# Kernel tuning notes

Measured on AMD Instinct MI355X. Metric: run time of the kernel, lower is better.

The kernel has to match this reference:

```python
import jax, jax.numpy as jnp
import numpy as np

DIM, NH, WS, SR, CTS = 256, 8, 8, 4, 2
HD = DIM // NH
SCALE = HD ** -0.5

def _linear(x, w, b=None):
    y = x @ w.T
    return y + b if b is not None else y

def _ln(x, g, b, eps=1e-5):
    m = jnp.mean(x, -1, keepdims=True)
    v = jnp.mean((x - m) ** 2, -1, keepdims=True)
    return (x - m) / jnp.sqrt(v + eps) * g + b

def _mlp(x, w1, b1, w2, b2):
    return _linear(jax.nn.gelu(_linear(x, w1, b1), approximate=False), w2, b2)

def _pos_emb_rank3(seq_len, w1, b1, w2):
    # PosEmbMLPSwinv1D with rank=3: coords on cube_root(seq) grid, normalized
    s = int(round(seq_len ** (1.0 / 3.0)))
    c = (jnp.arange(s, dtype=jnp.float32) - s // 2) / (s // 2)
    grid = jnp.stack(jnp.meshgrid(c, c, c, indexing='ij'))      # (3,s,s,s)
    tbl = grid.reshape(3, -1).T                                 # (s^3,3)
    return _linear(jax.nn.relu(_linear(tbl, w1, b1)), w2)[None]  # (1,s^3,dim)

def _rel_bias_3d(ws, w1, b1, w2, n_global):
    # PosEmbMLPSwinv3D: CPB-MLP bias over 3D relative coords, 16*sigmoid, zero-pad for carrier tokens
    r = jnp.arange(-(ws - 1), ws, dtype=jnp.float32)
    tbl = jnp.stack(jnp.meshgrid(r, r, r, indexing='ij'), axis=-1) / (ws - 1)
    tbl = tbl * 8.0
    tbl = jnp.sign(tbl) * jnp.log2(jnp.abs(tbl) + 1.0) / np.log2(8.0)
    table = _linear(jax.nn.relu(_linear(tbl.reshape(-1, 3), w1, b1)), w2)  # ((2ws-1)^3, NH)
    coords = jnp.stack(jnp.meshgrid(jnp.arange(ws), jnp.arange(ws), jnp.arange(ws), indexing='ij'))
    cf = coords.reshape(3, -1)
    rel = (cf[:, :, None] - cf[:, None, :]).transpose(1, 2, 0) + (ws - 1)  # (P,P,3)
    idx = rel[..., 0] * (2 * ws - 1) ** 2 + rel[..., 1] * (2 * ws - 1) + rel[..., 2]
    P = ws ** 3
    bias = table[idx.reshape(-1)].reshape(P, P, NH).transpose(2, 0, 1)
    bias = 16.0 * jax.nn.sigmoid(bias)
    return jnp.pad(bias, ((0, 0), (n_global, 0), (n_global, 0)))[None]  # (1,NH,P+g,P+g)

def _win_attn(x, qkv_w, qkv_b, proj_w, proj_b, bias):
    B, N, C = x.shape
    qkv = _linear(x, qkv_w, qkv_b).reshape(B, N, 3, NH, HD).transpose(2, 0, 3, 1, 4)
    q, k, v = qkv[0], qkv[1], qkv[2]
    attn = jax.nn.softmax(jnp.einsum('bhnd,bhmd->bhnm', q, k) * SCALE + bias, axis=-1)
    out = jnp.einsum('bhnm,bhmd->bhnd', attn, v).transpose(0, 2, 1, 3).reshape(B, N, C)
    return _linear(out, proj_w, proj_b)

def _ct_dewindow(ct, W, H, D, ws):
    bs, _, N = ct.shape
    c = ct.reshape(bs, W // ws, H // ws, D // ws, ws, ws, ws, N)
    c = c.transpose(0, 7, 1, 3, 5, 2, 4, 6).reshape(bs, N, W * H * D)
    return c.transpose(0, 2, 1)

def _ct_window(ct, W, H, D, ws):
    bs, _, N = ct.shape
    c = ct.reshape(bs, H // ws, ws, W // ws, ws, D // ws, ws, N)
    return c.transpose(0, 1, 3, 5, 2, 4, 6, 7)

def setup_inputs() -> dict:
    key = jax.random.key(0)
    ks = jax.random.split(key, 48)
    B0 = 1
    nw = SR ** 3
    def w(k, *s):
        return jax.random.normal(k, s, jnp.float32) * 0.02
    def b(k, *s):
        return jax.random.normal(k, s, jnp.float32) * 0.01
    d4 = 4 * DIM
    return {
        'x': jax.random.normal(ks[0], (B0 * nw, WS ** 3, DIM), jnp.float32),
        'ct': jax.random.normal(ks[1], (B0, (CTS * SR) ** 3, DIM), jnp.float32),
        'pe_w1': w(ks[2], 512, 3), 'pe_b1': b(ks[3], 512), 'pe_w2': w(ks[4], DIM, 512),
        'hpe_w1': w(ks[5], 512, 3), 'hpe_b1': b(ks[6], 512), 'hpe_w2': w(ks[7], DIM, 512),
        'hat_n1_g': jnp.ones((DIM,), jnp.float32), 'hat_n1_b': jnp.zeros((DIM,), jnp.float32),
        'hat_qkv_w': w(ks[8], 3 * DIM, DIM), 'hat_qkv_b': b(ks[9], 3 * DIM),
        'hat_proj_w': w(ks[10], DIM, DIM), 'hat_proj_b': b(ks[11], DIM),
        'hat_cpb_w1': w(ks[12], 512, 3), 'hat_cpb_b1': b(ks[13], 512), 'hat_cpb_w2': w(ks[14], NH, 512),
        'hat_n2_g': jnp.ones((DIM,), jnp.float32), 'hat_n2_b': jnp.zeros((DIM,), jnp.float32),
        'hat_fc1_w': w(ks[15], d4, DIM), 'hat_fc1_b': b(ks[16], d4),
        'hat_fc2_w': w(ks[17], DIM, d4), 'hat_fc2_b': b(ks[18], DIM),
        'n1_g': jnp.ones((DIM,), jnp.float32), 'n1_b': jnp.zeros((DIM,), jnp.float32),
        'qkv_w': w(ks[19], 3 * DIM, DIM), 'qkv_b': b(ks[20], 3 * DIM),
        'proj_w': w(ks[21], DIM, DIM), 'proj_b': b(ks[22], DIM),
        'cpb_w1': w(ks[23], 512, 3), 'cpb_b1': b(ks[24], 512), 'cpb_w2': w(ks[25], NH, 512),
        'n2_g': jnp.ones((DIM,), jnp.float32), 'n2_b': jnp.zeros((DIM,), jnp.float32),
        'fc1_w': w(ks[26], d4, DIM), 'fc1_b': b(ks[27], d4),
        'fc2_w': w(ks[28], DIM, d4), 'fc2_b': b(ks[29], DIM),
    }

def reference(x, ct, pe_w1, pe_b1, pe_w2, hpe_w1, hpe_b1, hpe_w2,
              hat_n1_g, hat_n1_b, hat_qkv_w, hat_qkv_b, hat_proj_w, hat_proj_b,
              hat_cpb_w1, hat_cpb_b1, hat_cpb_w2, hat_n2_g, hat_n2_b,
              hat_fc1_w, hat_fc1_b, hat_fc2_w, hat_fc2_b,
              n1_g, n1_b, qkv_w, qkv_b, proj_w, proj_b,
              cpb_w1, cpb_b1, cpb_w2, n2_g, n2_b, fc1_w, fc1_b, fc2_w, fc2_b):
    Bg, Ng, Hg = ct.shape
    G = CTS * SR  # carrier-token global cube side
    x = x + _pos_emb_rank3(x.shape[1], pe_w1, pe_b1, pe_w2)
    # carrier-token global attention (hierarchical path)
    ct = _ct_dewindow(ct, G, G, G, CTS)
    ct = ct + _pos_emb_rank3(ct.shape[1], hpe_w1, hpe_b1, hpe_w2)
    hat_bias = _rel_bias_3d(G, hat_cpb_w1, hat_cpb_b1, hat_cpb_w2, 0)
    ct = ct + _win_attn(_ln(ct, hat_n1_g, hat_n1_b), hat_qkv_w, hat_qkv_b, hat_proj_w, hat_proj_b, hat_bias)
    ct = ct + _mlp(_ln(ct, hat_n2_g, hat_n2_b), hat_fc1_w, hat_fc1_b, hat_fc2_w, hat_fc2_b)
    ct_w = _ct_window(ct, G, G, G, CTS).reshape(x.shape[0], -1, Hg)
    # windowed attention over [carrier tokens ; window tokens]
    x = jnp.concatenate([ct_w, x], axis=1)
    bias = _rel_bias_3d(WS, cpb_w1, cpb_b1, cpb_w2, CTS ** 3)
    x = x + _win_attn(_ln(x, n1_g, n1_b), qkv_w, qkv_b, proj_w, proj_b, bias)
    x = x + _mlp(_ln(x, n2_g, n2_b), fc1_w, fc1_b, fc2_w, fc2_b)
    split = x.shape[1] - WS ** 3
    ctr, x = x[:, :split], x[:, split:]
    return x, ctr.reshape(Bg, Ng, Hg)
```

## Files before the change

kernel.cpp:

```cpp
#include <hip/hip_runtime.h>
#include <hip/hip_bf16.h>
#include <math.h>

typedef __hip_bfloat16 bf16;

#define SCALE_QK 0.17677669529663687f

__device__ __forceinline__ float b2f(bf16 v){ return __bfloat162float(v); }
__device__ __forceinline__ bf16  f2b(float v){ return __float2bfloat16(v); }
__device__ __forceinline__ short bfs(float x){ bf16 b = f2b(x); short s; __builtin_memcpy(&s, &b, 2); return s; }

struct __align__(16) bf16x8 { bf16 v[8]; };
struct __align__(8)  bf16x4 { bf16 v[4]; };

typedef __attribute__((ext_vector_type(8))) short sh8;
typedef __attribute__((ext_vector_type(4))) short sh4;
typedef __attribute__((ext_vector_type(4))) float f4;

#if defined(__has_builtin)
#if __has_builtin(__builtin_amdgcn_mfma_f32_16x16x16bf16_1k)
#define HAS_MFMA16 1
#else
#define HAS_MFMA16 0
#endif
// ... 64 lines not shown
    int i = t / 225, r = t - i * 225, j = r / 15, k = r - j * 15;
    float x0 = cpb_coord(i), x1 = cpb_coord(j), x2 = cpb_coord(k);
    float h = x0 * w1[tid*3+0] + x1 * w1[tid*3+1] + x2 * w1[tid*3+2] + b1[tid];
    hid[tid] = fmaxf(h, 0.f);
    __syncthreads();
    int h8 = tid >> 6, lane = tid & 63;
    float p = 0.f;
    for (int jj = lane; jj < 512; jj += 64) p += hid[jj] * w2[h8*512 + jj];
    for (int off = 32; off; off >>= 1) p += __shfl_down(p, off);
    if (lane == 0) tab[t * 8 + h8] = p;
}

__global__ __launch_bounds__(256) void biasbuild_k(const float* __restrict__ taba, float* __restrict__ biasQa,
                                                   const float* __restrict__ tabb, float* __restrict__ biasQb) {
    const float* tab = blockIdx.y ? tabb : taba;
    float* biasQ     = blockIdx.y ? biasQb : biasQa;
    int idx = blockIdx.x * 256 + threadIdx.x;
    int h = idx >> 18, rem = idx & 262143;
    int q = rem >> 9, k = rem & 511;
    int qx = q >> 6, qy = (q >> 3) & 7, qz = q & 7;
    int kx = k >> 6, ky = (k >> 3) & 7, kz = k & 7;
    int tidx = ((qx - kx + 7) * 15 + (qy - ky + 7)) * 15 + (qz - kz + 7);
    float v = tab[tidx * 8 + h];
    float b = 16.f / (1.f + __expf(-v));
    biasQ[idx] = (b - 24.0f) * 1.4426950408889634f;
}

__global__ __launch_bounds__(256) void ct0ln_k(const float* __restrict__ ct_in,
                                               const float* __restrict__ hpe,
                                               const float* __restrict__ g,
                                               const float* __restrict__ b,
                                               float* __restrict__ ct0,
                                               bf16* __restrict__ lnout) {
    int u = blockIdx.x, c = threadIdx.x;
    int a = u >> 7, cc = (u >> 5) & 3, e = (u >> 4) & 1, bb = (u >> 2) & 3, d = (u >> 1) & 1, f = u & 1;
    int t = a * 128 + bb * 32 + cc * 8 + d * 4 + e * 2 + f;
    float x = ct_in[(size_t)t * 256 + c] + hpe[(size_t)u * 256 + c];
    ct0[(size_t)u * 256 + c] = x;
    float s = x, s2 = x * x;
    for (int off = 32; off; off >>= 1) { s += __shfl_down(s, off); s2 += __shfl_down(s2, off); }
    __shared__ float red[8];
    int wid = c >> 6, lane = c & 63;
    if (lane == 0) { red[wid] = s; red[wid + 4] = s2; }
    __syncthreads();
    if (c == 0) { red[0] = red[0] + red[1] + red[2] + red[3]; red[4] = red[4] + red[5] + red[6] + red[7]; }
    __syncthreads();
    float mean = red[0] * (1.f / 256.f);
    float var  = fmaxf(red[4] * (1.f / 256.f) - mean * mean, 0.f);
    float rstd = rsqrtf(var + 1e-5f);
    lnout[(size_t)u * 256 + c] = f2b((x - mean) * rstd * g[c] + b[c]);
}

__global__ __launch_bounds__(256) void ln_k(const float* __restrict__ in,
                                            const float* __restrict__ g,
                                            const float* __restrict__ b,
                                            bf16* __restrict__ out) {
    int row = blockIdx.x, c = threadIdx.x;
    float x = in[(size_t)row * 256 + c];
    float s = x, s2 = x * x;
    for (int off = 32; off; off >>= 1) { s += __shfl_down(s, off); s2 += __shfl_down(s2, off); }
    __shared__ float red[8];
    int wid = c >> 6, lane = c & 63;
    if (lane == 0) { red[wid] = s; red[wid + 4] = s2; }
    __syncthreads();
    if (c == 0) { red[0] = red[0] + red[1] + red[2] + red[3]; red[4] = red[4] + red[5] + red[6] + red[7]; }
    __syncthreads();
    float mean = red[0] * (1.f / 256.f);
    float var  = fmaxf(red[4] * (1.f / 256.f) - mean * mean, 0.f);
    float rstd = rsqrtf(var + 1e-5f);
    out[(size_t)row * 256 + c] = f2b((x - mean) * rstd * g[c] + b[c]);
}

template <int MODE>
__global__ __launch_bounds__(256) void gemm_k(const bf16* __restrict__ A,
                                              const bf16* __restrict__ W,
                                              const float* __restrict__ bias,
                                              int M, int N, int K,
                                              float* __restrict__ res,
                                              bf16* __restrict__ outb) {
    __shared__ short As[128 * 40];
    __shared__ short Ws[128 * 40];
    int m0 = blockIdx.y * 128, n0 = blockIdx.x * 128;
    int tid = threadIdx.x;
    int lane = tid & 63, wave = tid >> 6;
    int quad = lane >> 4, m16 = lane & 15;
    int wm = (wave & 1) * 64, wn = (wave >> 1) * 64;
    int arow = tid >> 2, acol = (tid & 3) * 8;

    f4 acc[4][4];
    #pragma unroll
    for (int i = 0; i < 4; i++)
        #pragma unroll
        for (int j = 0; j < 4; j++) acc[i][j] = (f4){0.f, 0.f, 0.f, 0.f};

    for (int k0 = 0; k0 < K; k0 += 32) {
        sh8 a0 = *reinterpret_cast<const sh8*>(A + (size_t)(m0 + arow) * K + k0 + acol);
        sh8 a1 = *reinterpret_cast<const sh8*>(A + (size_t)(m0 + arow + 64) * K + k0 + acol);
        sh8 w0 = *reinterpret_cast<const sh8*>(W + (size_t)(n0 + arow) * K + k0 + acol);
        sh8 w1 = *reinterpret_cast<const sh8*>(W + (size_t)(n0 + arow + 64) * K + k0 + acol);
        __syncthreads();
        *reinterpret_cast<sh8*>(&As[arow * 40 + acol])        = a0;
        *reinterpret_cast<sh8*>(&As[(arow + 64) * 40 + acol]) = a1;
        *reinterpret_cast<sh8*>(&Ws[arow * 40 + acol])        = w0;
        *reinterpret_cast<sh8*>(&Ws[(arow + 64) * 40 + acol]) = w1;
        __syncthreads();
        sh8 af[4], bf[4];
        #pragma unroll
        for (int mi = 0; mi < 4; mi++)
            af[mi] = *reinterpret_cast<const sh8*>(&As[(wm + mi * 16 + m16) * 40 + quad * 8]);
        #pragma unroll
        for (int ni = 0; ni < 4; ni++)
            bf[ni] = *reinterpret_cast<const sh8*>(&Ws[(wn + ni * 16 + m16) * 40 + quad * 8]);
        #pragma unroll
        for (int mi = 0; mi < 4; mi++)
            #pragma unroll
            for (int ni = 0; ni < 4; ni++)
                acc[mi][ni] = __builtin_amdgcn_mfma_f32_16x16x32_bf16(af[mi], bf[ni], acc[mi][ni], 0, 0, 0);
    }
    (void)M;

    #pragma unroll
    for (int mi = 0; mi < 4; mi++) {
        #pragma unroll
        for (int r = 0; r < 4; r++) {
            int gm = m0 + wm + mi * 16 + quad * 4 + r;
            #pragma unroll
            for (int ni = 0; ni < 4; ni++) {
                int gn = n0 + wn + ni * 16 + m16;
                float v = acc[mi][ni][r];
                if constexpr (MODE != 3) v += bias[gn];
                if constexpr (MODE == 2)      res[(size_t)gm * N + gn] += v;
                else if constexpr (MODE == 3) res[(size_t)gm * N + gn] = v;
                else if constexpr (MODE == 1) outb[(size_t)gm * N + gn] = f2b(0.5f * v * (1.0f + erff(v * 0.70710678118654752f)));
                else                          outb[(size_t)gm * N + gn] = f2b(v);
            }
        }
    }
}

__global__ __launch_bounds__(512) void gemmln_k(const bf16* __restrict__ A,
                                                const bf16* __restrict__ W,
                                                const float* __restrict__ bias,
                                                float* __restrict__ xcat,
                                                const float* __restrict__ g,
                                                const float* __restrict__ b,
                                                bf16* __restrict__ outb) {
    __shared__ short As[128 * 40];
    __shared__ short Ws[256 * 40];
    __shared__ float redS[128 * 4];
    __shared__ float redQ[128 * 4];
    __shared__ float stat[128 * 2];
    int m0 = blockIdx.x * 128;
    int tid = threadIdx.x;
    int lane = tid & 63, wave = tid >> 6;
    int quad = lane >> 4, m16 = lane & 15;
    int wm = (wave >> 2) * 64, wn = (wave & 3) * 64;
    int arow = tid >> 2, acol = (tid & 3) * 8;

    f4 acc[4][4];
    #pragma unroll
    for (int i = 0; i < 4; i++)
        #pragma unroll
        for (int j = 0; j < 4; j++) acc[i][j] = (f4){0.f, 0.f, 0.f, 0.f};

    for (int k0 = 0; k0 < 256; k0 += 32) {
        sh8 a0 = *reinterpret_cast<const sh8*>(A + (size_t)(m0 + arow) * 256 + k0 + acol);
        sh8 w0 = *reinterpret_cast<const sh8*>(W + (size_t)arow * 256 + k0 + acol);
        sh8 w1 = *reinterpret_cast<const sh8*>(W + (size_t)(arow + 128) * 256 + k0 + acol);
        __syncthreads();
        *reinterpret_cast<sh8*>(&As[arow * 40 + acol])         = a0;
        *reinterpret_cast<sh8*>(&Ws[arow * 40 + acol])         = w0;
        *reinterpret_cast<sh8*>(&Ws[(arow + 128) * 40 + acol]) = w1;
        __syncthreads();
        sh8 af[4], bf[4];
        #pragma unroll
        for (int mi = 0; mi < 4; mi++)
            af[mi] = *reinterpret_cast<const sh8*>(&As[(wm + mi * 16 + m16) * 40 + quad * 8]);
        #pragma unroll
        for (int ni = 0; ni < 4; ni++)
            bf[ni] = *reinterpret_cast<const sh8*>(&Ws[(wn + ni * 16 + m16) * 40 + quad * 8]);
        #pragma unroll
        for (int mi = 0; mi < 4; mi++)
            #pragma unroll
            for (int ni = 0; ni < 4; ni++)
                acc[mi][ni] = __builtin_amdgcn_mfma_f32_16x16x32_bf16(af[mi], bf[ni], acc[mi][ni], 0, 0, 0);
    }

    #pragma unroll
    for (int mi = 0; mi < 4; mi++) {
        #pragma unroll
        for (int r = 0; r < 4; r++) {
            int lr = wm + mi * 16 + quad * 4 + r;
            int gm = m0 + lr;
            float ps = 0.f, pq = 0.f;
            #pragma unroll
            for (int ni = 0; ni < 4; ni++) {
                int gc = wn + ni * 16 + m16;
                float v = acc[mi][ni][r] + bias[gc] + xcat[(size_t)gm * 256 + gc];
                acc[mi][ni][r] = v;
                ps += v; pq += v * v;
            }
            ps += __shfl_xor(ps, 1); pq += __shfl_xor(pq, 1);
            ps += __shfl_xor(ps, 2); pq += __shfl_xor(pq, 2);
            ps += __shfl_xor(ps, 4); pq += __shfl_xor(pq, 4);
            ps += __shfl_xor(ps, 8); pq += __shfl_xor(pq, 8);
            if (m16 == 0) { redS[lr * 4 + (wave & 3)] = ps; redQ[lr * 4 + (wave & 3)] = pq; }
        }
    }
    __syncthreads();
    if (tid < 128) {
        float s = redS[tid * 4] + redS[tid * 4 + 1] + redS[tid * 4 + 2] + redS[tid * 4 + 3];
        float q = redQ[tid * 4] + redQ[tid * 4 + 1] + redQ[tid * 4 + 2] + redQ[tid * 4 + 3];
        float mean = s * (1.f / 256.f);
        float var  = fmaxf(q * (1.f / 256.f) - mean * mean, 0.f);
        stat[tid * 2]     = mean;
        stat[tid * 2 + 1] = rsqrtf(var + 1e-5f);
    }
    __syncthreads();
    #pragma unroll
    for (int mi = 0; mi < 4; mi++) {
        #pragma unroll
        for (int r = 0; r < 4; r++) {
            int lr = wm + mi * 16 + quad * 4 + r;
            int gm = m0 + lr;
            float mean = stat[lr * 2], rstd = stat[lr * 2 + 1];
            #pragma unroll
            for (int ni = 0; ni < 4; ni++) {
                int gc = wn + ni * 16 + m16;
                float v = acc[mi][ni][r];
                xcat[(size_t)gm * 256 + gc] = v;
                outb[(size_t)gm * 256 + gc] = f2b((v - mean) * rstd * g[gc] + b[gc]);
            }
        }
    }
}

__global__ __launch_bounds__(256) void gemmsplit_k(const bf16* __restrict__ A,
                                                   const bf16* __restrict__ W,
                                                   const float* __restrict__ bias,
                                                   int K,
                                                   const float* __restrict__ res,
                                                   float* __restrict__ out) {
    __shared__ short As[128 * 40];
    __shared__ short Ws[128 * 40];
    int m0 = blockIdx.y * 128, n0 = blockIdx.x * 128;
    int tid = threadIdx.x;
    int lane = tid & 63, wave = tid >> 6;
    int quad = lane >> 4, m16 = lane & 15;
    int wm = (wave & 1) * 64, wn = (wave >> 1) * 64;
    int arow = tid >> 2, acol = (tid & 3) * 8;

    f4 acc[4][4];
    #pragma unroll
    for (int i = 0; i < 4; i++)
        #pragma unroll
        for (int j = 0; j < 4; j++) acc[i][j] = (f4){0.f, 0.f, 0.f, 0.f};

    for (int k0 = 0; k0 < K; k0 += 32) {
        sh8 a0 = *reinterpret_cast<const sh8*>(A + (size_t)(m0 + arow) * K + k0 + acol);
        sh8 a1 = *reinterpret_cast<const sh8*>(A + (size_t)(m0 + arow + 64) * K + k0 + acol);
        sh8 w0 = *reinterpret_cast<const sh8*>(W + (size_t)(n0 + arow) * K + k0 + acol);
        sh8 w1 = *reinterpret_cast<const sh8*>(W + (size_t)(n0 + arow + 64) * K + k0 + acol);
        __syncthreads();
        *reinterpret_cast<sh8*>(&As[arow * 40 + acol])        = a0;
        *reinterpret_cast<sh8*>(&As[(arow + 64) * 40 + acol]) = a1;
        *reinterpret_cast<sh8*>(&Ws[arow * 40 + acol])        = w0;
        *reinterpret_cast<sh8*>(&Ws[(arow + 64) * 40 + acol]) = w1;
        __syncthreads();
        sh8 af[4], bf[4];
        #pragma unroll
        for (int mi = 0; mi < 4; mi++)
            af[mi] = *reinterpret_cast<const sh8*>(&As[(wm + mi * 16 + m16) * 40 + quad * 8]);
        #pragma unroll
        for (int ni = 0; ni < 4; ni++)
            bf[ni] = *reinterpret_cast<const sh8*>(&Ws[(wn + ni * 16 + m16) * 40 + quad * 8]);
        #pragma unroll
        for (int mi = 0; mi < 4; mi++)
            #pragma unroll
            for (int ni = 0; ni < 4; ni++)
                acc[mi][ni] = __builtin_amdgcn_mfma_f32_16x16x32_bf16(af[mi], bf[ni], acc[mi][ni], 0, 0, 0);
    }

    #pragma unroll
    for (int mi = 0; mi < 4; mi++) {
        #pragma unroll
        for (int r = 0; r < 4; r++) {
            int gm = m0 + wm + mi * 16 + quad * 4 + r;
            int w = gm / 520, p = gm - w * 520;
            size_t drow = (p >= 8) ? (size_t)(w * 512 + p - 8) : (size_t)(32768 + w * 8 + p);
            #pragma unroll
            for (int ni = 0; ni < 4; ni++) {
                int gn = n0 + wn + ni * 16 + m16;
                float v = acc[mi][ni][r] + bias[gn] + res[(size_t)gm * 256 + gn];
                out[drow * 256 + gn] = v;
            }
        }
    }
}

#define VSTR 548
#define SC2   0.25503575360579045f
#define CNB  (-34.62468098133512f)
#define NEGB (-1.0e30f)
__global__ __launch_bounds__(512) void flash_k(const bf16* __restrict__ qkv,
                                               const float* __restrict__ biasQ,
                                               bf16* __restrict__ out,
                                               int N, int glob) {
    int wh = blockIdx.x, w = wh >> 3, h = wh & 7;
    int qs = blockIdx.y, QS = gridDim.y;
    int tid = threadIdx.x;
    int lane = tid & 63, wave = tid >> 6;
    int quad = lane >> 4, qcol = lane & 15;
    const int NT32 = (N + 31) & ~31;

    __shared__ bf16 Vt[32 * VSTR];
#if !HAS_MFMA16
    __shared__ float Ps[8][16 * 17];
#endif

    for (int i = tid; i < NT32 * 4; i += 512) {
        int tok = i >> 2, seg = i & 3;
        if (tok < N) {
            const bf16* vp = qkv + ((size_t)(w * N + tok)) * 768 + 512 + h * 32 + seg * 8;
            bf16x8 vv = *reinterpret_cast<const bf16x8*>(vp);
            #pragma unroll
            for (int e = 0; e < 8; e++) Vt[(seg * 8 + e) * VSTR + tok] = vv.v[e];
        } else {
            bf16 z = f2b(0.f);
            #pragma unroll
            for (int e = 0; e < 8; e++) Vt[(seg * 8 + e) * VSTR + tok] = z;
        }
    }
    __syncthreads();

    const bf16* qbase = qkv + ((size_t)w * N) * 768 + h * 32;
    const bf16* kbase = qbase + 256;
    int nqt = (N + 15) >> 4, nkt = NT32 >> 5;
    int nun = (nqt + 1) >> 1;

    for (int u = wave * QS + qs; u < nun; u += 8 * QS) {
        bool hasB = (2 * u + 1 < nqt);
        int qA = u * 32 + qcol;
        int qB = qA + 16;
        int qrA = (qA < N) ? qA : (N - 1);
        int qrB = (qB < N) ? qB : (N - 1);
        sh8 qfA = *reinterpret_cast<const sh8*>(qbase + (size_t)qrA * 768 + quad * 8);
        sh8 qfB = *reinterpret_cast<const sh8*>(qbase + (size_t)qrB * 768 + quad * 8);
        f4 O0A = {0.f,0.f,0.f,0.f}, O1A = {0.f,0.f,0.f,0.f};
        f4 O0B = {0.f,0.f,0.f,0.f}, O1B = {0.f,0.f,0.f,0.f};
        float lA = 0.f, lB = 0.f;
        bool vA = (qA >= glob) && (qA < N);
        bool vB = (qB >= glob) && (qB < N);
        const float* browA = biasQ + (((size_t)h << 9) + (size_t)(vA ? (qA - glob) : 0)) * 512 - glob;
        const float* browB = biasQ + (((size_t)h << 9) + (size_t)(vB ? (qB - glob) : 0)) * 512 - glob;

        sh8 kf0, kf1;
        {
            int k0 = qcol, k1 = 16 + qcol;
            kf0 = *reinterpret_cast<const sh8*>(kbase + (size_t)((k0 < N) ? k0 : (N - 1)) * 768 + quad * 8);
            kf1 = *reinterpret_cast<const sh8*>(kbase + (size_t)((k1 < N) ? k1 : (N - 1)) * 768 + quad * 8);
        }

        for (int kt = 0; kt < nkt; kt++) {
            int bt = kt * 32;
            sh8 c0 = kf0, c1 = kf1;
            if (kt + 1 < nkt) {
                int n0 = bt + 32 + qcol, n1 = bt + 48 + qcol;
                kf0 = *reinterpret_cast<const sh8*>(kbase + (size_t)((n0 < N) ? n0 : (N - 1)) * 768 + quad * 8);
                kf1 = *reinterpret_cast<const sh8*>(kbase + (size_t)((n1 < N) ? n1 : (N - 1)) * 768 + quad * 8);
            }
            f4 z = {0.f, 0.f, 0.f, 0.f};
            f4 s0A = __builtin_amdgcn_mfma_f32_16x16x32_bf16(c0, qfA, z, 0, 0, 0);
            f4 s1A = __builtin_amdgcn_mfma_f32_16x16x32_bf16(c1, qfA, z, 0, 0, 0);
            f4 s0B = z, s1B = z;
            if (hasB) {
                s0B = __builtin_amdgcn_mfma_f32_16x16x32_bf16(c0, qfB, z, 0, 0, 0);
                s1B = __builtin_amdgcn_mfma_f32_16x16x32_bf16(c1, qfB, z, 0, 0, 0);
            }

            int tg0 = bt + quad * 4, tg1 = bt + 16 + quad * 4;
            bool val0 = tg0 < N, val1 = tg1 < N;
            f4 bb0A, bb1A;
            if (!val0)                    bb0A = (f4){NEGB, NEGB, NEGB, NEGB};
            else if (vA && tg0 >= glob)   bb0A = *reinterpret_cast<const f4*>(browA + tg0);
            else                          bb0A = (f4){CNB, CNB, CNB, CNB};
            if (!val1)                    bb1A = (f4){NEGB, NEGB, NEGB, NEGB};
            else if (vA && tg1 >= glob)   bb1A = *reinterpret_cast<const f4*>(browA + tg1);
            else                          bb1A = (f4){CNB, CNB, CNB, CNB};

            float pA[8];
            #pragma unroll
            for (int r = 0; r < 4; r++) {
                pA[r]     = EXP2(fmaf(s0A[r], SC2, bb0A[r]));
                pA[4 + r] = EXP2(fmaf(s1A[r], SC2, bb1A[r]));
            }
            #pragma unroll
            for (int r = 0; r < 8; r++) lA += pA[r];

            float pB[8];
            if (hasB) {
                f4 bb0B, bb1B;
                if (!val0)                    bb0B = (f4){NEGB, NEGB, NEGB, NEGB};
                else if (vB && tg0 >= glob)   bb0B = *reinterpret_cast<const f4*>(browB + tg0);
                else                          bb0B = (f4){CNB, CNB, CNB, CNB};
                if (!val1)                    bb1B = (f4){NEGB, NEGB, NEGB, NEGB};
                else if (vB && tg1 >= glob)   bb1B = *reinterpret_cast<const f4*>(browB + tg1);
                else                          bb1B = (f4){CNB, CNB, CNB, CNB};
                #pragma unroll
                for (int r = 0; r < 4; r++) {
                    pB[r]     = EXP2(fmaf(s0B[r], SC2, bb0B[r]));
                    pB[4 + r] = EXP2(fmaf(s1B[r], SC2, bb1B[r]));
                }
                #pragma unroll
                for (int r = 0; r < 8; r++) lB += pB[r];
            }

#if HAS_MFMA16
            sh4 v00 = *reinterpret_cast<const sh4*>(&Vt[qcol * VSTR + bt + quad * 4]);
            sh4 v10 = *reinterpret_cast<const sh4*>(&Vt[qcol * VSTR + bt + 16 + quad * 4]);
            sh4 v01 = *reinterpret_cast<const sh4*>(&Vt[(qcol + 16) * VSTR + bt + quad * 4]);
            sh4 v11 = *reinterpret_cast<const sh4*>(&Vt[(qcol + 16) * VSTR + bt + 16 + quad * 4]);
            sh4 pf0A, pf1A;
            #pragma unroll
            for (int r = 0; r < 4; r++) { pf0A[r] = bfs(pA[r]); pf1A[r] = bfs(pA[4 + r]); }
            O0A = __builtin_amdgcn_mfma_f32_16x16x16bf16_1k(v00, pf0A, O0A, 0, 0, 0);
            O0A = __builtin_amdgcn_mfma_f32_16x16x16bf16_1k(v10, pf1A, O0A, 0, 0, 0);
            O1A = __builtin_amdgcn_mfma_f32_16x16x16bf16_1k(v01, pf0A, O1A, 0, 0, 0);
            O1A = __builtin_amdgcn_mfma_f32_16x16x16bf16_1k(v11, pf1A, O1A, 0, 0, 0);
            if (hasB) {
                sh4 pf0B, pf1B;
                #pragma unroll
                for (int r = 0; r < 4; r++) { pf0B[r] = bfs(pB[r]); pf1B[r] = bfs(pB[4 + r]); }
                O0B = __builtin_amdgcn_mfma_f32_16x16x16bf16_1k(v00, pf0B, O0B, 0, 0, 0);
                O0B = __builtin_amdgcn_mfma_f32_16x16x16bf16_1k(v10, pf1B, O0B, 0, 0, 0);
                O1B = __builtin_amdgcn_mfma_f32_16x16x16bf16_1k(v01, pf0B, O1B, 0, 0, 0);
                O1B = __builtin_amdgcn_mfma_f32_16x16x16bf16_1k(v11, pf1B, O1B, 0, 0, 0);
            }
#else
            for (int t = 0; t < 2; t++) {
                if (t == 1 && !hasB) break;
                const float* ph = t ? pB : pA;
                for (int half = 0; half < 2; half++) {
                    #pragma unroll
                    for (int r = 0; r < 4; r++) Ps[wave][(quad * 4 + r) * 17 + qcol] = ph[half * 4 + r];
                    __builtin_amdgcn_wave_barrier();
                    sh8 pbig, va, vb;
                    #pragma unroll
                    for (int j = 0; j < 8; j++) {
                        int tl = quad * 8 + j;
                        float pv = (quad < 2) ? Ps[wave][tl * 17 + qcol] : 0.f;
                        pbig[j] = bfs(pv);
                        bf16 a0 = (quad < 2) ? Vt[qcol * VSTR + bt + half * 16 + tl] : f2b(0.f);
                        bf16 a1 = (quad < 2) ? Vt[(qcol + 16) * VSTR + bt + half * 16 + tl] : f2b(0.f);
                        short t0, t1;
                        __builtin_memcpy(&t0, &a0, 2); __builtin_memcpy(&t1, &a1, 2);
                        va[j] = t0; vb[j] = t1;
                    }
                    if (t == 0) {
                        O0A = __builtin_amdgcn_mfma_f32_16x16x32_bf16(va, pbig, O0A, 0, 0, 0);
                        O1A = __builtin_amdgcn_mfma_f32_16x16x32_bf16(vb, pbig, O1A, 0, 0, 0);
                    } else {
                        O0B = __builtin_amdgcn_mfma_f32_16x16x32_bf16(va, pbig, O0B, 0, 0, 0);
                        O1B = __builtin_amdgcn_mfma_f32_16x16x32_bf16(vb, pbig, O1B, 0, 0, 0);
                    }
                    __builtin_amdgcn_wave_barrier();
                }
            }
#endif
        }

        lA += __shfl_xor(lA, 16); lA += __shfl_xor(lA, 32);
        float rlA = 1.f / lA;
        if (qA < N) {
            bf16x4 o0, o1;
            #pragma unroll
            for (int r = 0; r < 4; r++) { o0.v[r] = f2b(O0A[r] * rlA); o1.v[r] = f2b(O1A[r] * rlA); }
            bf16* op = out + ((size_t)(w * N + qA)) * 256 + h * 32 + quad * 4;
            *reinterpret_cast<bf16x4*>(op)      = o0;
            *reinterpret_cast<bf16x4*>(op + 16) = o1;
        }
        if (hasB) {
            lB += __shfl_xor(lB, 16); lB += __shfl_xor(lB, 32);
            float rlB = 1.f / lB;
            if (qB < N) {
                bf16x4 o0, o1;
                #pragma unroll
                for (int r = 0; r < 4; r++) { o0.v[r] = f2b(O0B[r] * rlB); o1.v[r] = f2b(O1B[r] * rlB); }
                bf16* op = out + ((size_t)(w * N + qB)) * 256 + h * 32 + quad * 4;
                *reinterpret_cast<bf16x4*>(op)      = o0;
                *reinterpret_cast<bf16x4*>(op + 16) = o1;
            }
        }
    }
}

__global__ __launch_bounds__(256) void xcatln_k(const float* __restrict__ x_in,
                                                const float* __restrict__ pe,
                                                const float* __restrict__ ct2,
                                                const float* __restrict__ g,
                                                const float* __restrict__ b,
                                                float* __restrict__ xcat,
                                                bf16* __restrict__ xln) {
    int row = blockIdx.x, w = row / 520, p = row - w * 520, c = threadIdx.x;
    float v;
    if (p < 8) {
        int P = w >> 4, Q = (w >> 2) & 3, R = w & 3;
        int S = p >> 2, T = (p >> 1) & 1, U = p & 1;
        int t = P * 128 + S * 64 + Q * 16 + T * 8 + R * 2 + U;
        v = ct2[(size_t)t * 256 + c];
    } else {
        int t = p - 8;
        v = x_in[((size_t)w * 512 + t) * 256 + c] + pe[(size_t)t * 256 + c];
    }
    xcat[(size_t)row * 256 + c] = v;
    float s = v, s2 = v * v;
    for (int off = 32; off; off >>= 1) { s += __shfl_down(s, off); s2 += __shfl_down(s2, off); }
    __shared__ float red[8];
    int wid = c >> 6, lane = c & 63;
    if (lane == 0) { red[wid] = s; red[wid + 4] = s2; }
    __syncthreads();
    if (c == 0) { red[0] = red[0] + red[1] + red[2] + red[3]; red[4] = red[4] + red[5] + red[6] + red[7]; }
    __syncthreads();
    float mean = red[0] * (1.f / 256.f);
    float var  = fmaxf(red[4] * (1.f / 256.f) - mean * mean, 0.f);
    float rstd = rsqrtf(var + 1e-5f);
    xln[(size_t)row * 256 + c] = f2b((v - mean) * rstd * g[c] + b[c]);
}

__global__ __launch_bounds__(256) void xcatbuild_k(const float* __restrict__ x_in,
                                                   const float* __restrict__ pe,
                                                   const float* __restrict__ ct2,
                                                   float* __restrict__ xcat) {
    int row = blockIdx.x, w = row / 520, p = row - w * 520, c = threadIdx.x;
    float v;
    if (p < 8) {
        int P = w >> 4, Q = (w >> 2) & 3, R = w & 3;
        int S = p >> 2, T = (p >> 1) & 1, U = p & 1;
        int t = P * 128 + S * 64 + Q * 16 + T * 8 + R * 2 + U;
        v = ct2[(size_t)t * 256 + c];
    } else {
        int t = p - 8;
        v = x_in[((size_t)w * 512 + t) * 256 + c] + pe[(size_t)t * 256 + c];
    }
    xcat[(size_t)row * 256 + c] = v;
}

__global__ __launch_bounds__(256) void outbuild_k(const float* __restrict__ xcat,
                                                  float* __restrict__ out) {
    int row = blockIdx.x, w = row / 520, p = row - w * 520, c = threadIdx.x;
    float v = xcat[(size_t)row * 256 + c];
    if (p >= 8) out[((size_t)(w * 512) + (p - 8)) * 256 + c] = v;
    else        out[(size_t)8388608 + ((size_t)(w * 8) + p) * 256 + c] = v;
}

extern "C" void kernel_launch(void* const* d_in, const int* in_sizes, int n_in,
                              void* d_out, int out_size, void* d_ws, size_t ws_size,
                              hipStream_t stream) {
    const float* x          = (const float*)d_in[0];
    const float* ct         = (const float*)d_in[1];
    const float* pe_w1      = (const float*)d_in[2];
    const float* pe_b1      = (const float*)d_in[3];
    const float* pe_w2      = (const float*)d_in[4];
    const float* hpe_w1     = (const float*)d_in[5];
    const float* hpe_b1     = (const float*)d_in[6];
    const float* hpe_w2     = (const float*)d_in[7];
    const float* hat_n1_g   = (const float*)d_in[8];
    const float* hat_n1_b   = (const float*)d_in[9];
    const float* hat_qkv_w  = (const float*)d_in[10];
    const float* hat_qkv_b  = (const float*)d_in[11];
    const float* hat_proj_w = (const float*)d_in[12];
    const float* hat_proj_b = (const float*)d_in[13];
    const float* hat_cpb_w1 = (const float*)d_in[14];
    const float* hat_cpb_b1 = (const float*)d_in[15];
    const float* hat_cpb_w2 = (const float*)d_in[16];
    const float* hat_n2_g   = (const float*)d_in[17];
    const float* hat_n2_b   = (const float*)d_in[18];
    const float* hat_fc1_w  = (const float*)d_in[19];
    const float* hat_fc1_b  = (const float*)d_in[20];
    const float* hat_fc2_w  = (const float*)d_in[21];
    const float* hat_fc2_b  = (const float*)d_in[22];
    const float* n1_g       = (const float*)d_in[23];
    const float* n1_b       = (const float*)d_in[24];
    const float* qkv_w      = (const float*)d_in[25];
    const float* qkv_b      = (const float*)d_in[26];
    const float* proj_w     = (const float*)d_in[27];
    const float* proj_b     = (const float*)d_in[28];
    const float* cpb_w1     = (const float*)d_in[29];
    const float* cpb_b1     = (const float*)d_in[30];
    const float* cpb_w2     = (const float*)d_in[31];
    const float* n2_g       = (const float*)d_in[32];
    const float* n2_b       = (const float*)d_in[33];
    const float* fc1_w      = (const float*)d_in[34];
    const float* fc1_b      = (const float*)d_in[35];
    const float* fc2_w      = (const float*)d_in[36];
    const float* fc2_b      = (const float*)d_in[37];
    (void)in_sizes; (void)n_in; (void)out_size;

    char* base = (char*)d_ws;
    size_t off = 0;
    auto alloc = [&](size_t bytes) -> void* {
        void* p = base + off;
        off += (bytes + 255) & ~(size_t)255;
        return p;
    };
    float* pe        = (float*)alloc(512 * 256 * 4);
    float* hpe       = (float*)alloc(512 * 256 * 4);
    float* tab_hat   = (float*)alloc(3375 * 8 * 4);
    float* tab2      = (float*)alloc(3375 * 8 * 4);
    float* biasQ2    = (float*)alloc((size_t)8 * 512 * 512 * 4);
    float* ct0       = (float*)alloc(512 * 256 * 4);
    bf16* wb_hqkv  = (bf16*)alloc(768 * 256 * 2);
    bf16* wb_hproj = (bf16*)alloc(256 * 256 * 2);
    bf16* wb_hfc1  = (bf16*)alloc(1024 * 256 * 2);
    bf16* wb_hfc2  = (bf16*)alloc(256 * 1024 * 2);
    bf16* wb_qkv   = (bf16*)alloc(768 * 256 * 2);
    bf16* wb_proj  = (bf16*)alloc(256 * 256 * 2);
    bf16* wb_fc1   = (bf16*)alloc(1024 * 256 * 2);
    bf16* wb_fc2   = (bf16*)alloc(256 * 1024 * 2);
    bf16* wb_pew2  = (bf16*)alloc(256 * 512 * 2);
    bf16* wb_hpew2 = (bf16*)alloc(256 * 512 * 2);
    size_t zstart = off;
    bf16*  hidA      = (bf16*)alloc(512 * 512 * 2);
    bf16*  hidB      = (bf16*)alloc(512 * 512 * 2);
    off = zstart;
    float* biasQ_hat = (float*)alloc((size_t)8 * 512 * 512 * 4);
    bf16*  hct_ln    = (bf16*)alloc(512 * 256 * 2);
    bf16*  hqkv      = (bf16*)alloc(512 * 768 * 2);
    bf16*  hat_attn  = (bf16*)alloc(512 * 256 * 2);
    bf16*  hat_hid   = (bf16*)alloc(512 * 1024 * 2);
    off = zstart;
    float* xcat      = (float*)alloc((size_t)64 * 520 * 256 * 4);
    const int S     = (ws_size >= (size_t)150 * 1024 * 1024) ? 1 : 4;
    const int rows  = 33280 / S;
    const int wins  = 64 / S;
    bf16*  xln_b     = (bf16*)alloc((size_t)rows * 256 * 2);
    char*  region_qa = (char*)alloc((size_t)rows * 1024 * 2);
    bf16*  qkv_b_    = (bf16*)region_qa;
    bf16*  attn_b    = (bf16*)(region_qa + (size_t)rows * 768 * 2);
    bf16*  hidden    = (bf16*)region_qa;

    wcvt10_k<<<dim3(1024, 10), 256, 0, stream>>>(hat_qkv_w, hat_proj_w, hat_fc1_w, hat_fc2_w,
                                                 qkv_w, proj_w, fc1_w, fc2_w, pe_w2, hpe_w2,
                                                 wb_hqkv, wb_hproj, wb_hfc1, wb_hfc2,
                                                 wb_qkv, wb_proj, wb_fc1, wb_fc2, wb_pew2, wb_hpew2);

    hidbuild_k<<<dim3(512, 2), 256, 0, stream>>>(pe_w1, pe_b1, hpe_w1, hpe_b1, hidA, hidB);
    gemm_k<3><<<dim3(2, 4), 256, 0, stream>>>(hidA, wb_pew2,  nullptr, 512, 256, 512, pe,  nullptr);
    gemm_k<3><<<dim3(2, 4), 256, 0, stream>>>(hidB, wb_hpew2, nullptr, 512, 256, 512, hpe, nullptr);

    cpbtab_k<<<dim3(3375, 2), 512, 0, stream>>>(hat_cpb_w1, hat_cpb_b1, hat_cpb_w2, tab_hat,
                                                cpb_w1, cpb_b1, cpb_w2, tab2);
    biasbuild_k<<<dim3(8192, 2), 256, 0, stream>>>(tab_hat, biasQ_hat, tab2, biasQ2);

    ct0ln_k<<<512, 256, 0, stream>>>(ct, hpe, hat_n1_g, hat_n1_b, ct0, hct_ln);
    gemm_k<0><<<dim3(6, 4), 256, 0, stream>>>(hct_ln, wb_hqkv, hat_qkv_b, 512, 768, 256, nullptr, hqkv);
    flash_k<<<dim3(8, 2), 512, 0, stream>>>(hqkv, biasQ_hat, hat_attn, 512, 0);
    gemmln_k<<<4, 512, 0, stream>>>(hat_attn, wb_hproj, hat_proj_b, ct0, hat_n2_g, hat_n2_b, hct_ln);
    gemm_k<1><<<dim3(8, 4), 256, 0, stream>>>(hct_ln, wb_hfc1, hat_fc1_b, 512, 1024, 256, nullptr, hat_hid);
    gemm_k<2><<<dim3(2, 4), 256, 0, stream>>>(hat_hid, wb_hfc2, hat_fc2_b, 512, 256, 1024, ct0, nullptr);

    if (S == 1) {
        xcatln_k<<<33280, 256, 0, stream>>>(x, pe, ct0, n1_g, n1_b, xcat, xln_b);
        gemm_k<0><<<dim3(6, 260), 256, 0, stream>>>(xln_b, wb_qkv, qkv_b, 33280, 768, 256, nullptr, qkv_b_);
        flash_k<<<dim3(512, 2), 512, 0, stream>>>(qkv_b_, biasQ2, attn_b, 520, 8);
        gemmln_k<<<260, 512, 0, stream>>>(attn_b, wb_proj, proj_b, xcat, n2_g, n2_b, xln_b);
        gemm_k<1><<<dim3(8, 260), 256, 0, stream>>>(xln_b, wb_fc1, fc1_b, 33280, 1024, 256, nullptr, hidden);
        gemmsplit_k<<<dim3(2, 260), 256, 0, stream>>>(hidden, wb_fc2, fc2_b, 1024, xcat, (float*)d_out);
    } else {
        xcatbuild_k<<<33280, 256, 0, stream>>>(x, pe, ct0, xcat);
        for (int s = 0; s < S; s++) {
            float* xc = xcat + (size_t)s * rows * 256;
            ln_k<<<rows, 256, 0, stream>>>(xc, n1_g, n1_b, xln_b);
            gemm_k<0><<<dim3(6, rows / 128), 256, 0, stream>>>(xln_b, wb_qkv, qkv_b, rows, 768, 256, nullptr, qkv_b_);
            flash_k<<<dim3(wins * 8, 2), 512, 0, stream>>>(qkv_b_, biasQ2, attn_b, 520, 8);
            gemm_k<2><<<dim3(2, rows / 128), 256, 0, stream>>>(attn_b, wb_proj, proj_b, rows, 256, 256, xc, nullptr);
        }
        for (int s = 0; s < S; s++) {
            float* xc = xcat + (size_t)s * rows * 256;
            ln_k<<<rows, 256, 0, stream>>>(xc, n2_g, n2_b, xln_b);
            gemm_k<1><<<dim3(8, rows / 128), 256, 0, stream>>>(xln_b, wb_fc1, fc1_b, rows, 1024, 256, nullptr, hidden);
            gemm_k<2><<<dim3(2, rows / 128), 256, 0, stream>>>(hidden, wb_fc2, fc2_b, rows, 256, 1024, xc, nullptr);
        }
        outbuild_k<<<33280, 256, 0, stream>>>(xcat, (float*)d_out);
    }
}
```

Baseline: 605.8 us.

## Use one 1024-thread block per window-head in flash attention, split-K the odd query tile

The flash attention kernel moves from two 512-thread blocks per window-head, which each load V into shared memory, to a single 1024-thread block with 16 waves. V is now loaded once per window-head. The main loop handles only full pairs of 16-row query tiles, so the hasB branches and row clamps are gone. When the tile count is odd, the last 16-row tile is split across all waves along the key axis, and partial outputs and sums are combined through shared memory with a block barrier. In exchange the grid has half as many blocks, waves per block double, shared memory use grows with the reduction buffer, and the odd tile adds a synchronisation.

New measurement: 763.7 us. +26.1%, slower.

```diff
diff --git a/kernel.cpp b/kernel.cpp
--- a/kernel.cpp
+++ b/kernel.cpp
@@ -390,23 +390,24 @@
 #define SC2   0.25503575360579045f
 #define CNB  (-34.62468098133512f)
 #define NEGB (-1.0e30f)
-__global__ __launch_bounds__(512) void flash_k(const bf16* __restrict__ qkv,
-                                               const float* __restrict__ biasQ,
-                                               bf16* __restrict__ out,
-                                               int N, int glob) {
+#define FW 16
+__global__ __launch_bounds__(1024, 8) void flash_k(const bf16* __restrict__ qkv,
+                                                   const float* __restrict__ biasQ,
+                                                   bf16* __restrict__ out,
+                                                   int N, int glob) {
     int wh = blockIdx.x, w = wh >> 3, h = wh & 7;
-    int qs = blockIdx.y, QS = gridDim.y;
     int tid = threadIdx.x;
     int lane = tid & 63, wave = tid >> 6;
     int quad = lane >> 4, qcol = lane & 15;
     const int NT32 = (N + 31) & ~31;
 
     __shared__ bf16 Vt[32 * VSTR];
+    __shared__ float red[FW][64][9];
 #if !HAS_MFMA16
-    __shared__ float Ps[8][16 * 17];
+    __shared__ float Ps[FW][16 * 17];
 #endif
 
-    for (int i = tid; i < NT32 * 4; i += 512) {
+    for (int i = tid; i < NT32 * 4; i += 1024) {
         int tok = i >> 2, seg = i & 3;
         if (tok < N) {
             const bf16* vp = qkv + ((size_t)(w * N + tok)) * 768 + 512 + h * 32 + seg * 8;
@@ -424,21 +425,19 @@
     const bf16* qbase = qkv + ((size_t)w * N) * 768 + h * 32;
     const bf16* kbase = qbase + 256;
     int nqt = (N + 15) >> 4, nkt = NT32 >> 5;
-    int nun = (nqt + 1) >> 1;
-
-    for (int u = wave * QS + qs; u < nun; u += 8 * QS) {
-        bool hasB = (2 * u + 1 < nqt);
+    int nfull = nqt >> 1;
+    bool hasRunt = (nqt & 1) != 0;
+
+    for (int u = wave; u < nfull; u += FW) {
         int qA = u * 32 + qcol;
         int qB = qA + 16;
-        int qrA = (qA < N) ? qA : (N - 1);
-        int qrB = (qB < N) ? qB : (N - 1);
-        sh8 qfA = *reinterpret_cast<const sh8*>(qbase + (size_t)qrA * 768 + quad * 8);
-        sh8 qfB = *reinterpret_cast<const sh8*>(qbase + (size_t)qrB * 768 + quad * 8);
+        sh8 qfA = *reinterpret_cast<const sh8*>(qbase + (size_t)qA * 768 + quad * 8);
+        sh8 qfB = *reinterpret_cast<const sh8*>(qbase + (size_t)qB * 768 + quad * 8);
         f4 O0A = {0.f,0.f,0.f,0.f}, O1A = {0.f,0.f,0.f,0.f};
         f4 O0B = {0.f,0.f,0.f,0.f}, O1B = {0.f,0.f,0.f,0.f};
         float lA = 0.f, lB = 0.f;
-        bool vA = (qA >= glob) && (qA < N);
-        bool vB = (qB >= glob) && (qB < N);
+        bool vA = (qA >= glob);
+        bool vB = (qB >= glob);
         const float* browA = biasQ + (((size_t)h << 9) + (size_t)(vA ? (qA - glob) : 0)) * 512 - glob;
         const float* browB = biasQ + (((size_t)h << 9) + (size_t)(vB ? (qB - glob) : 0)) * 512 - glob;
 
@@ -460,73 +459,57 @@
             f4 z = {0.f, 0.f, 0.f, 0.f};
             f4 s0A = __builtin_amdgcn_mfma_f32_16x16x32_bf16(c0, qfA, z, 0, 0, 0);
             f4 s1A = __builtin_amdgcn_mfma_f32_16x16x32_bf16(c1, qfA, z, 0, 0, 0);
-            f4 s0B = z, s1B = z;
-            if (hasB) {
-                s0B = __builtin_amdgcn_mfma_f32_16x16x32_bf16(c0, qfB, z, 0, 0, 0);
-                s1B = __builtin_amdgcn_mfma_f32_16x16x32_bf16(c1, qfB, z, 0, 0, 0);
-            }
+            f4 s0B = __builtin_amdgcn_mfma_f32_16x16x32_bf16(c0, qfB, z, 0, 0, 0);
+            f4 s1B = __builtin_amdgcn_mfma_f32_16x16x32_bf16(c1, qfB, z, 0, 0, 0);
 
             int tg0 = bt + quad * 4, tg1 = bt + 16 + quad * 4;
             bool val0 = tg0 < N, val1 = tg1 < N;
-            f4 bb0A, bb1A;
+            f4 bb0A, bb1A, bb0B, bb1B;
             if (!val0)                    bb0A = (f4){NEGB, NEGB, NEGB, NEGB};
             else if (vA && tg0 >= glob)   bb0A = *reinterpret_cast<const f4*>(browA + tg0);
             else                          bb0A = (f4){CNB, CNB, CNB, CNB};
             if (!val1)                    bb1A = (f4){NEGB, NEGB, NEGB, NEGB};
             else if (vA && tg1 >= glob)   bb1A = *reinterpret_cast<const f4*>(browA + tg1);
             else                          bb1A = (f4){CNB, CNB, CNB, CNB};
-
-            float pA[8];
+            if (!val0)                    bb0B = (f4){NEGB, NEGB, NEGB, NEGB};
+            else if (vB && tg0 >= glob)   bb0B = *reinterpret_cast<const f4*>(browB + tg0);
+            else                          bb0B = (f4){CNB, CNB, CNB, CNB};
+            if (!val1)                    bb1B = (f4){NEGB, NEGB, NEGB, NEGB};
+            else if (vB && tg1 >= glob)   bb1B = *reinterpret_cast<const f4*>(browB + tg1);
+            else                          bb1B = (f4){CNB, CNB, CNB, CNB};
+
+            float pA[8], pB[8];
             #pragma unroll
             for (int r = 0; r < 4; r++) {
                 pA[r]     = EXP2(fmaf(s0A[r], SC2, bb0A[r]));
                 pA[4 + r] = EXP2(fmaf(s1A[r], SC2, bb1A[r]));
-            }
-            #pragma unroll
-            for (int r = 0; r < 8; r++) lA += pA[r];
-
-            float pB[8];
-            if (hasB) {
-                f4 bb0B, bb1B;
-                if (!val0)                    bb0B = (f4){NEGB, NEGB, NEGB, NEGB};
-                else if (vB && tg0 >= glob)   bb0B = *reinterpret_cast<const f4*>(browB + tg0);
-                else                          bb0B = (f4){CNB, CNB, CNB, CNB};
-                if (!val1)                    bb1B = (f4){NEGB, NEGB, NEGB, NEGB};
-                else if (vB && tg1 >= glob)   bb1B = *reinterpret_cast<const f4*>(browB + tg1);
-                else                          bb1B = (f4){CNB, CNB, CNB, CNB};
-                #pragma unroll
-                for (int r = 0; r < 4; r++) {
-                    pB[r]     = EXP2(fmaf(s0B[r], SC2, bb0B[r]));
-                    pB[4 + r] = EXP2(fmaf(s1B[r], SC2, bb1B[r]));
-                }
-                #pragma unroll
-                for (int r = 0; r < 8; r++) lB += pB[r];
-            }
+                pB[r]     = EXP2(fmaf(s0B[r], SC2, bb0B[r]));
+                pB[4 + r] = EXP2(fmaf(s1B[r], SC2, bb1B[r]));
+            }
+            #pragma unroll
+            for (int r = 0; r < 8; r++) { lA += pA[r]; lB += pB[r]; }
 
 #if HAS_MFMA16
             sh4 v00 = *reinterpret_cast<const sh4*>(&Vt[qcol * VSTR + bt + quad * 4]);
             sh4 v10 = *reinterpret_cast<const sh4*>(&Vt[qcol * VSTR + bt + 16 + quad * 4]);
             sh4 v01 = *reinterpret_cast<const sh4*>(&Vt[(qcol + 16) * VSTR + bt + quad * 4]);
             sh4 v11 = *reinterpret_cast<const sh4*>(&Vt[(qcol + 16) * VSTR + bt + 16 + quad * 4]);
-            sh4 pf0A, pf1A;
-            #pragma unroll
-            for (int r = 0; r < 4; r++) { pf0A[r] = bfs(pA[r]); pf1A[r] = bfs(pA[4 + r]); }
+            sh4 pf0A, pf1A, pf0B, pf1B;
+            #pragma unroll
+            for (int r = 0; r < 4; r++) {
+                pf0A[r] = bfs(pA[r]); pf1A[r] = bfs(pA[4 + r]);
+                pf0B[r] = bfs(pB[r]); pf1B[r] = bfs(pB[4 + r]);
+            }
             O0A = __builtin_amdgcn_mfma_f32_16x16x16bf16_1k(v00, pf0A, O0A, 0, 0, 0);
             O0A = __builtin_amdgcn_mfma_f32_16x16x16bf16_1k(v10, pf1A, O0A, 0, 0, 0);
             O1A = __builtin_amdgcn_mfma_f32_16x16x16bf16_1k(v01, pf0A, O1A, 0, 0, 0);
             O1A = __builtin_amdgcn_mfma_f32_16x16x16bf16_1k(v11, pf1A, O1A, 0, 0, 0);
-            if (hasB) {
-                sh4 pf0B, pf1B;
-                #pragma unroll
-                for (int r = 0; r < 4; r++) { pf0B[r] = bfs(pB[r]); pf1B[r] = bfs(pB[4 + r]); }
-                O0B = __builtin_amdgcn_mfma_f32_16x16x16bf16_1k(v00, pf0B, O0B, 0, 0, 0);
-                O0B = __builtin_amdgcn_mfma_f32_16x16x16bf16_1k(v10, pf1B, O0B, 0, 0, 0);
-                O1B = __builtin_amdgcn_mfma_f32_16x16x16bf16_1k(v01, pf0B, O1B, 0, 0, 0);
-                O1B = __builtin_amdgcn_mfma_f32_16x16x16bf16_1k(v11, pf1B, O1B, 0, 0, 0);
-            }
+            O0B = __builtin_amdgcn_mfma_f32_16x16x16bf16_1k(v00, pf0B, O0B, 0, 0, 0);
+            O0B = __builtin_amdgcn_mfma_f32_16x16x16bf16_1k(v10, pf1B, O0B, 0, 0, 0);
+            O1B = __builtin_amdgcn_mfma_f32_16x16x16bf16_1k(v01, pf0B, O1B, 0, 0, 0);
+            O1B = __builtin_amdgcn_mfma_f32_16x16x16bf16_1k(v11, pf1B, O1B, 0, 0, 0);
 #else
             for (int t = 0; t < 2; t++) {
-                if (t == 1 && !hasB) break;
                 const float* ph = t ? pB : pA;
                 for (int half = 0; half < 2; half++) {
                     #pragma unroll
@@ -558,8 +541,9 @@
         }
 
         lA += __shfl_xor(lA, 16); lA += __shfl_xor(lA, 32);
-        float rlA = 1.f / lA;
-        if (qA < N) {
+        lB += __shfl_xor(lB, 16); lB += __shfl_xor(lB, 32);
+        float rlA = 1.f / lA, rlB = 1.f / lB;
+        {
             bf16x4 o0, o1;
             #pragma unroll
             for (int r = 0; r < 4; r++) { o0.v[r] = f2b(O0A[r] * rlA); o1.v[r] = f2b(O1A[r] * rlA); }
@@ -567,14 +551,110 @@
             *reinterpret_cast<bf16x4*>(op)      = o0;
             *reinterpret_cast<bf16x4*>(op + 16) = o1;
         }
-        if (hasB) {
-            lB += __shfl_xor(lB, 16); lB += __shfl_xor(lB, 32);
-            float rlB = 1.f / lB;
-            if (qB < N) {
+        {
+            bf16x4 o0, o1;
+            #pragma unroll
+            for (int r = 0; r < 4; r++) { o0.v[r] = f2b(O0B[r] * rlB); o1.v[r] = f2b(O1B[r] * rlB); }
+            bf16* op = out + ((size_t)(w * N + qB)) * 256 + h * 32 + quad * 4;
+            *reinterpret_cast<bf16x4*>(op)      = o0;
+            *reinterpret_cast<bf16x4*>(op + 16) = o1;
+        }
+    }
+
+    if (hasRunt) {
+        int rt = nfull * 2;
+        int qA = rt * 16 + qcol;
+        int qrA = (qA < N) ? qA : (N - 1);
+        sh8 qfA = *reinterpret_cast<const sh8*>(qbase + (size_t)qrA * 768 + quad * 8);
+        f4 O0 = {0.f,0.f,0.f,0.f}, O1 = {0.f,0.f,0.f,0.f};
+        float l = 0.f;
+        bool vA = (qA >= glob) && (qA < N);
+        const float* browA = biasQ + (((size_t)h << 9) + (size_t)(vA ? (qA - glob) : 0)) * 512 - glob;
+
+        for (int kt = wave; kt < nkt; kt += FW) {
+            int bt = kt * 32;
+            int k0 = bt + qcol, k1 = bt + 16 + qcol;
+            sh8 c0 = *reinterpret_cast<const sh8*>(kbase + (size_t)((k0 < N) ? k0 : (N - 1)) * 768 + quad * 8);
+            sh8 c1 = *reinterpret_cast<const sh8*>(kbase + (size_t)((k1 < N) ? k1 : (N - 1)) * 768 + quad * 8);
+            f4 z = {0.f, 0.f, 0.f, 0.f};
+            f4 s0 = __builtin_amdgcn_mfma_f32_16x16x32_bf16(c0, qfA, z, 0, 0, 0);
+            f4 s1 = __builtin_amdgcn_mfma_f32_16x16x32_bf16(c1, qfA, z, 0, 0, 0);
+
+            int tg0 = bt + quad * 4, tg1 = bt + 16 + quad * 4;
+            bool val0 = tg0 < N, val1 = tg1 < N;
+            f4 bb0, bb1;
+            if (!val0)                    bb0 = (f4){NEGB, NEGB, NEGB, NEGB};
+            else if (vA && tg0 >= glob)   bb0 = *reinterpret_cast<const f4*>(browA + tg0);
+            else                          bb0 = (f4){CNB, CNB, CNB, CNB};
+            if (!val1)                    bb1 = (f4){NEGB, NEGB, NEGB, NEGB};
+            else if (vA && tg1 >= glob)   bb1 = *reinterpret_cast<const f4*>(browA + tg1);
+            else                          bb1 = (f4){CNB, CNB, CNB, CNB};
+
+            float p[8];
+            #pragma unroll
+            for (int r = 0; r < 4; r++) {
+                p[r]     = EXP2(fmaf(s0[r], SC2, bb0[r]));
+                p[4 + r] = EXP2(fmaf(s1[r], SC2, bb1[r]));
+            }
+            #pragma unroll
+            for (int r = 0; r < 8; r++) l += p[r];
+
+#if HAS_MFMA16
+            sh4 v00 = *reinterpret_cast<const sh4*>(&Vt[qcol * VSTR + bt + quad * 4]);
+            sh4 v10 = *reinterpret_cast<const sh4*>(&Vt[qcol * VSTR + bt + 16 + quad * 4]);
+            sh4 v01 = *reinterpret_cast<const sh4*>(&Vt[(qcol + 16) * VSTR + bt + quad * 4]);
+            sh4 v11 = *reinterpret_cast<const sh4*>(&Vt[(qcol + 16) * VSTR + bt + 16 + quad * 4]);
+            sh4 pf0, pf1;
+            #pragma unroll
+            for (int r = 0; r < 4; r++) { pf0[r] = bfs(p[r]); pf1[r] = bfs(p[4 + r]); }
+            O0 = __builtin_amdgcn_mfma_f32_16x16x16bf16_1k(v00, pf0, O0, 0, 0, 0);
+            O0 = __builtin_amdgcn_mfma_f32_16x16x16bf16_1k(v10, pf1, O0, 0, 0, 0);
+            O1 = __builtin_amdgcn_mfma_f32_16x16x16bf16_1k(v01, pf0, O1, 0, 0, 0);
+            O1 = __builtin_amdgcn_mfma_f32_16x16x16bf16_1k(v11, pf1, O1, 0, 0, 0);
+#else
+            for (int half = 0; half < 2; half++) {
+                #pragma unroll
+                for (int r = 0; r < 4; r++) Ps[wave][(quad * 4 + r) * 17 + qcol] = p[half * 4 + r];
+                __builtin_amdgcn_wave_barrier();
+                sh8 pbig, va, vb;
+                #pragma unroll
+                for (int j = 0; j < 8; j++) {
+                    int tl = quad * 8 + j;
+                    float pv = (quad < 2) ? Ps[wave][tl * 17 + qcol] : 0.f;
+                    pbig[j] = bfs(pv);
+                    bf16 a0 = (quad < 2) ? Vt[qcol * VSTR + bt + half * 16 + tl] : f2b(0.f);
+                    bf16 a1 = (quad < 2) ? Vt[(qcol + 16) * VSTR + bt + half * 16 + tl] : f2b(0.f);
+                    short t0, t1;
+                    __builtin_memcpy(&t0, &a0, 2); __builtin_memcpy(&t1, &a1, 2);
+                    va[j] = t0; vb[j] = t1;
+                }
+                O0 = __builtin_amdgcn_mfma_f32_16x16x32_bf16(va, pbig, O0, 0, 0, 0);
+                O1 = __builtin_amdgcn_mfma_f32_16x16x32_bf16(vb, pbig, O1, 0, 0, 0);
+                __builtin_amdgcn_wave_barrier();
+            }
+#endif
+        }
+
+        #pragma unroll
+        for (int r = 0; r < 4; r++) { red[wave][lane][r] = O0[r]; red[wave][lane][4 + r] = O1[r]; }
+        red[wave][lane][8] = l;
+        __syncthreads();
+
+        if (wave == 0) {
+            f4 O0s = {0.f,0.f,0.f,0.f}, O1s = {0.f,0.f,0.f,0.f};
+            float ls = 0.f;
+            for (int v = 0; v < FW; v++) {
+                #pragma unroll
+                for (int r = 0; r < 4; r++) { O0s[r] += red[v][lane][r]; O1s[r] += red[v][lane][4 + r]; }
+                ls += red[v][lane][8];
+            }
+            ls += __shfl_xor(ls, 16); ls += __shfl_xor(ls, 32);
+            float rl = 1.f / ls;
+            if (qA < N) {
                 bf16x4 o0, o1;
                 #pragma unroll
-                for (int r = 0; r < 4; r++) { o0.v[r] = f2b(O0B[r] * rlB); o1.v[r] = f2b(O1B[r] * rlB); }
-                bf16* op = out + ((size_t)(w * N + qB)) * 256 + h * 32 + quad * 4;
+                for (int r = 0; r < 4; r++) { o0.v[r] = f2b(O0s[r] * rl); o1.v[r] = f2b(O1s[r] * rl); }
+                bf16* op = out + ((size_t)(w * N + qA)) * 256 + h * 32 + quad * 4;
                 *reinterpret_cast<bf16x4*>(op)      = o0;
                 *reinterpret_cast<bf16x4*>(op + 16) = o1;
             }
@@ -742,7 +822,7 @@
 
     ct0ln_k<<<512, 256, 0, stream>>>(ct, hpe, hat_n1_g, hat_n1_b, ct0, hct_ln);
     gemm_k<0><<<dim3(6, 4), 256, 0, stream>>>(hct_ln, wb_hqkv, hat_qkv_b, 512, 768, 256, nullptr, hqkv);
-    flash_k<<<dim3(8, 2), 512, 0, stream>>>(hqkv, biasQ_hat, hat_attn, 512, 0);
+    flash_k<<<8, 1024, 0, stream>>>(hqkv, biasQ_hat, hat_attn, 512, 0);
     gemmln_k<<<4, 512, 0, stream>>>(hat_attn, wb_hproj, hat_proj_b, ct0, hat_n2_g, hat_n2_b, hct_ln);
     gemm_k<1><<<dim3(8, 4), 256, 0, stream>>>(hct_ln, wb_hfc1, hat_fc1_b, 512, 1024, 256, nullptr, hat_hid);
     gemm_k<2><<<dim3(2, 4), 256, 0, stream>>>(hat_hid, wb_hfc2, hat_fc2_b, 512, 256, 1024, ct0, nullptr);
@@ -750,7 +830,7 @@
     if (S == 1) {
         xcatln_k<<<33280, 256, 0, stream>>>(x, pe, ct0, n1_g, n1_b, xcat, xln_b);
         gemm_k<0><<<dim3(6, 260), 256, 0, stream>>>(xln_b, wb_qkv, qkv_b, 33280, 768, 256, nullptr, qkv_b_);
-        flash_k<<<dim3(512, 2), 512, 0, stream>>>(qkv_b_, biasQ2, attn_b, 520, 8);
+        flash_k<<<512, 1024, 0, stream>>>(qkv_b_, biasQ2, attn_b, 520, 8);
         gemmln_k<<<260, 512, 0, stream>>>(attn_b, wb_proj, proj_b, xcat, n2_g, n2_b, xln_b);
         gemm_k<1><<<dim3(8, 260), 256, 0, stream>>>(xln_b, wb_fc1, fc1_b, 33280, 1024, 256, nullptr, hidden);
         gemmsplit_k<<<dim3(2, 260), 256, 0, stream>>>(hidden, wb_fc2, fc2_b, 1024, xcat, (float*)d_out);
@@ -760,7 +840,7 @@
             float* xc = xcat + (size_t)s * rows * 256;
             ln_k<<<rows, 256, 0, stream>>>(xc, n1_g, n1_b, xln_b);
             gemm_k<0><<<dim3(6, rows / 128), 256, 0, stream>>>(xln_b, wb_qkv, qkv_b, rows, 768, 256, nullptr, qkv_b_);
-            flash_k<<<dim3(wins * 8, 2), 512, 0, stream>>>(qkv_b_, biasQ2, attn_b, 520, 8);
+            flash_k<<<wins * 8, 1024, 0, stream>>>(qkv_b_, biasQ2, attn_b, 520, 8);
             gemm_k<2><<<dim3(2, rows / 128), 256, 0, stream>>>(attn_b, wb_proj, proj_b, rows, 256, 256, xc, nullptr);
         }
         for (int s = 0; s < S; s++) {
```
